# Performance work log

Measured on AMD Instinct MI355X. Metric: run time of the kernel, lower is better.

The kernel has to match this reference:

```python
import jax, jax.numpy as jnp
import numpy as np

ALPHA, BETA, GAMMA = 2.0, 2.0, 1.0
EPS = 1e-8  # torch F.cosine_similarity eps
B, T, D = 64, 1024, 256


def setup_inputs() -> dict:
    key = jax.random.key(0)
    k1, k2, k3 = jax.random.split(key, 3)
    f_v = jax.random.normal(k1, (B, T, D), dtype=jnp.float32)
    f_a = jax.random.normal(k2, (B, T, D), dtype=jnp.float32)
    labels = jax.random.randint(k3, (B,), 0, 2, dtype=jnp.int64)
    return {"f_v": f_v, "f_a": f_a, "labels": labels}


def _normalize(x):
    n = jnp.sqrt(jnp.sum(x * x, axis=-1, keepdims=True))
    return x / jnp.maximum(n, EPS)


def reference(f_v, f_a, labels):
    b, t, _ = f_v.shape
    vn = _normalize(f_v)  # [B,T,D]
    an = _normalize(f_a)  # [B,T,D]

    # --- per-timestep aligned-pair term ---
    cos_bt = jnp.sum(vn * an, axis=-1)  # [B,T] cosine sim
    d_bt = 1.0 - cos_bt                  # cosine distance
    pos_mask = (labels == 0).astype(f_v.dtype)[:, None]  # [B,1]
    neg_mask = 1.0 - pos_mask
    loss_pos = ALPHA * jnp.sum(d_bt * pos_mask)
    cnt_pos = jnp.sum(pos_mask) * t
    loss_neg = BETA * jnp.sum((1.0 - d_bt) * neg_mask)  # (1-d) == cos
    cnt_neg = jnp.sum(neg_mask) * t

    # --- cross-sample term: for i != j, (1 - mean_t d_ij) = mean_t cos(v_i_t, a_j_t) ---
    cross_cos = jnp.einsum('itd,jtd->ij', vn, an) / t  # [B,B] mean over T
    offdiag = 1.0 - jnp.eye(b, dtype=f_v.dtype)
    loss_neg = loss_neg + GAMMA * jnp.sum(cross_cos * offdiag)
    cnt_neg = cnt_neg + b * (b - 1)

    loss = jnp.where(cnt_pos > 0, loss_pos / jnp.maximum(cnt_pos, 1.0), 0.0)
    loss = loss + jnp.where(cnt_neg > 0, loss_neg / jnp.maximum(cnt_neg, 1.0), 0.0)
    return loss
```

## Files before the change

### kernel.cpp

```cpp
#include <hip/hip_runtime.h>

constexpr int Bn = 64;
constexpr int Tn = 1024;
constexpr int Dn = 256;

constexpr int TPB  = 256;
constexpr int NBLK = Tn / 4;
constexpr int NBIN = 64;

using short8 = __attribute__((ext_vector_type(8))) short;
using f32x16 = __attribute__((ext_vector_type(16))) float;

__device__ __forceinline__ float dot4(const float4& a, const float4& b) {
    return a.x * b.x + a.y * b.y + a.z * b.z + a.w * b.w;
}

__device__ __forceinline__ unsigned int bfbits(float x) {
    unsigned int u = __builtin_bit_cast(unsigned int, x);
    return (u + 0x7FFFu + ((u >> 16) & 1u)) >> 16;
}
__device__ __forceinline__ unsigned int pack_bf2(float lo, float hi) {
    return bfbits(lo) | (bfbits(hi) << 16);
}

struct Ch { float4 v0[2], v1[2], a0[2], a1[2]; };

__global__ __launch_bounds__(TPB, 3)
void cmfm_main(const float* __restrict__ fv, const float* __restrict__ fa,
               const int* __restrict__ labels, float* __restrict__ acc)
{
    const int lane = threadIdx.x & 63;
    const int wave = threadIdx.x >> 6;
    const int t    = blockIdx.x * 4 + wave;

    const int mrow = lane & 31;
    const int half = lane >> 5;

    const size_t RS = (size_t)Tn * Dn;
    const float* pv0 = fv + ((size_t)mrow * Tn + t) * Dn + half * 8;
    const float* pv1 = pv0 + 32 * RS;
    const float* pa0 = fa + ((size_t)mrow * Tn + t) * Dn + half * 8;
    const float* pa1 = pa0 + 32 * RS;

    f32x16 C00, C01, C10, C11;
    #pragma unroll
    for (int r = 0; r < 16; ++r) { C00[r] = 0.f; C01[r] = 0.f; C10[r] = 0.f; C11[r] = 0.f; }

    float sqv0 = 0.f, sqv1 = 0.f, sqa0 = 0.f, sqa1 = 0.f, dva0 = 0.f, dva1 = 0.f;

    #define LOADC(ch, OFF) do {                                              \
        ch.v0[0] = *reinterpret_cast<const float4*>(pv0 + (OFF));            \
        ch.v0[1] = *reinterpret_cast<const float4*>(pv0 + (OFF) + 4);        \
        ch.v1[0] = *reinterpret_cast<const float4*>(pv1 + (OFF));            \
        ch.v1[1] = *reinterpret_cast<const float4*>(pv1 + (OFF) + 4);        \
        ch.a0[0] = *reinterpret_cast<const float4*>(pa0 + (OFF));            \
        ch.a0[1] = *reinterpret_cast<const float4*>(pa0 + (OFF) + 4);        \
        ch.a1[0] = *reinterpret_cast<const float4*>(pa1 + (OFF));            \
        ch.a1[1] = *reinterpret_cast<const float4*>(pa1 + (OFF) + 4);        \
    } while (0)

    #define CONSUME(ch) do {                                                 \
        sqv0 += dot4(ch.v0[0], ch.v0[0]) + dot4(ch.v0[1], ch.v0[1]);         \
        sqv1 += dot4(ch.v1[0], ch.v1[0]) + dot4(ch.v1[1], ch.v1[1]);         \
        sqa0 += dot4(ch.a0[0], ch.a0[0]) + dot4(ch.a0[1], ch.a0[1]);         \
        sqa1 += dot4(ch.a1[0], ch.a1[0]) + dot4(ch.a1[1], ch.a1[1]);         \
        dva0 += dot4(ch.v0[0], ch.a0[0]) + dot4(ch.v0[1], ch.a0[1]);         \
        dva1 += dot4(ch.v1[0], ch.a1[0]) + dot4(ch.v1[1], ch.a1[1]);         \
        union { short8 s8; uint4 u4; } vf0, vf1, af0, af1;                   \
        vf0.u4.x = pack_bf2(ch.v0[0].x, ch.v0[0].y);                         \
        vf0.u4.y = pack_bf2(ch.v0[0].z, ch.v0[0].w);                         \
        vf0.u4.z = pack_bf2(ch.v0[1].x, ch.v0[1].y);                         \
        vf0.u4.w = pack_bf2(ch.v0[1].z, ch.v0[1].w);                         \
        vf1.u4.x = pack_bf2(ch.v1[0].x, ch.v1[0].y);                         \
        vf1.u4.y = pack_bf2(ch.v1[0].z, ch.v1[0].w);                         \
        vf1.u4.z = pack_bf2(ch.v1[1].x, ch.v1[1].y);                         \
        vf1.u4.w = pack_bf2(ch.v1[1].z, ch.v1[1].w);                         \
        af0.u4.x = pack_bf2(ch.a0[0].x, ch.a0[0].y);                         \
        af0.u4.y = pack_bf2(ch.a0[0].z, ch.a0[0].w);                         \
        af0.u4.z = pack_bf2(ch.a0[1].x, ch.a0[1].y);                         \
        af0.u4.w = pack_bf2(ch.a0[1].z, ch.a0[1].w);                         \
        af1.u4.x = pack_bf2(ch.a1[0].x, ch.a1[0].y);                         \
        af1.u4.y = pack_bf2(ch.a1[0].z, ch.a1[0].w);                         \
        af1.u4.z = pack_bf2(ch.a1[1].x, ch.a1[1].y);                         \
        af1.u4.w = pack_bf2(ch.a1[1].z, ch.a1[1].w);                         \
        C00 = __builtin_amdgcn_mfma_f32_32x32x16_bf16(vf0.s8, af0.s8, C00, 0, 0, 0); \
        C01 = __builtin_amdgcn_mfma_f32_32x32x16_bf16(vf0.s8, af1.s8, C01, 0, 0, 0); \
        C10 = __builtin_amdgcn_mfma_f32_32x32x16_bf16(vf1.s8, af0.s8, C10, 0, 0, 0); \
        C11 = __builtin_amdgcn_mfma_f32_32x32x16_bf16(vf1.s8, af1.s8, C11, 0, 0, 0); \
    } while (0)

    Ch cA, cB;
    LOADC(cA, 0);
    #pragma unroll 1
    for (int c = 0; c < Dn / 16; c += 2) {
        LOADC(cB, (c + 1) * 16);
        CONSUME(cA);
        if (c + 2 < Dn / 16) LOADC(cA, (c + 2) * 16);
        CONSUME(cB);
    }
    #undef LOADC
    #undef CONSUME

    sqv0 += __shfl_xor(sqv0, 32);  sqv1 += __shfl_xor(sqv1, 32);
    sqa0 += __shfl_xor(sqa0, 32);  sqa1 += __shfl_xor(sqa1, 32);
    dva0 += __shfl_xor(dva0, 32);  dva1 += __shfl_xor(dva1, 32);
    const float rv0 = 1.f / fmaxf(sqrtf(sqv0), 1e-8f);
    const float rv1 = 1.f / fmaxf(sqrtf(sqv1), 1e-8f);
    const float ra0 = 1.f / fmaxf(sqrtf(sqa0), 1e-8f);
    const float ra1 = 1.f / fmaxf(sqrtf(sqa1), 1e-8f);

    float pos = 0.f, neg = 0.f;
    if (half == 0) {
        const float c0 = dva0 * rv0 * ra0;
        const float c1 = dva1 * rv1 * ra1;
        if (labels[mrow] == 0)      pos += 1.f - c0; else neg += c0;
        if (labels[mrow + 32] == 0) pos += 1.f - c1; else neg += c1;
    }

    float od = 0.f;
    #define TILE(Cxx, RV, RA, EXCL) do {                                     \
        _Pragma("unroll")                                                    \
        for (int r = 0; r < 16; ++r) {                                       \
            const int ri = (r & 3) + 8 * (r >> 2) + 4 * half;                \
            const float rvi = __shfl(RV, ri);                                \
            float cc = Cxx[r];                                               \
            if (EXCL && ri == mrow) cc = 0.f;                                \
            od += rvi * (RA) * cc;                                           \
        }                                                                    \
    } while (0)
    TILE(C00, rv0, ra0, true);
    TILE(C01, rv0, ra1, false);
    TILE(C10, rv1, ra0, false);
    TILE(C11, rv1, ra1, true);
    #undef TILE

    #pragma unroll
    for (int off = 1; off < 64; off <<= 1) {
        pos += __shfl_xor(pos, off);
        neg += __shfl_xor(neg, off);
        od  += __shfl_xor(od, off);
    }
    if (lane == 0) {
        float* bin = acc + (size_t)(t & (NBIN - 1)) * 4;
        atomicAdd(bin + 0, pos);
        atomicAdd(bin + 1, neg);
        atomicAdd(bin + 2, od);
    }
}

__global__ void cmfm_final(const int* __restrict__ labels, const float* __restrict__ acc,
                           float* __restrict__ out) {
    const int l = threadIdx.x;
    float p = acc[l * 4 + 0];
    float n = acc[l * 4 + 1];
    float o = acc[l * 4 + 2];
    float npf = (labels[l] == 0) ? 1.f : 0.f;
    #pragma unroll
    for (int off = 1; off < 64; off <<= 1) {
        p += __shfl_xor(p, off);
        n += __shfl_xor(n, off);
        o += __shfl_xor(o, off);
        npf += __shfl_xor(npf, off);
    }
    if (l == 0) {
        const int np = (int)(npf + 0.5f);
        const float cnt_pos = (float)np * (float)Tn;
        const float cnt_neg = (float)(Bn - np) * (float)Tn + (float)Bn * (float)(Bn - 1);
        float loss = 0.f;
        if (np > 0) loss += 2.0f * p / cnt_pos;
        loss += (2.0f * n + 1.0f * o / (float)Tn) / cnt_neg;
        out[0] = loss;
    }
}

extern "C" void kernel_launch(void* const* d_in, const int* in_sizes, int n_in,
                              void* d_out, int out_size, void* d_ws, size_t ws_size,
                              hipStream_t stream) {
    const float* fv     = (const float*)d_in[0];
    const float* fa     = (const float*)d_in[1];
    const int*   labels = (const int*)d_in[2];
    float* acc = (float*)d_ws;
    float* out = (float*)d_out;

    hipMemsetAsync(acc, 0, NBIN * 4 * sizeof(float), stream);
    cmfm_main<<<NBLK, TPB, 0, stream>>>(fv, fa, labels, acc);
    cmfm_final<<<1, 64, 0, stream>>>(labels, acc, out);
}
```

Before: 169.7 us.

## Split D reduction across four waves per timestep, combine norms via shared memory

Each block now handles a single timestep, and its four waves each take a 64-wide slice of the feature dimension instead of each wave owning a whole timestep. Partial squared norms and dot products go to shared memory and are summed there. Each wave then applies the combined norms to its partial cross-sample MFMA tile, and the block reduces the results before the atomic adds. This gives four times as many blocks and shorter per-wave dependency chains to raise parallelism and latency hiding, at the cost of two block barriers and shared-memory traffic.

```diff
diff --git a/kernel.cpp b/kernel.cpp
--- a/kernel.cpp
+++ b/kernel.cpp
@@ -5,7 +5,7 @@
 constexpr int Dn = 256;
 
 constexpr int TPB  = 256;
-constexpr int NBLK = Tn / 4;
+constexpr int NBLK = Tn;
 constexpr int NBIN = 64;
 
 using short8 = __attribute__((ext_vector_type(8))) short;
@@ -29,17 +29,21 @@
 void cmfm_main(const float* __restrict__ fv, const float* __restrict__ fa,
                const int* __restrict__ labels, float* __restrict__ acc)
 {
+    __shared__ float nv[4][Bn], na[4][Bn], nd[4][Bn];
+    __shared__ float wred[3][4];
+
     const int lane = threadIdx.x & 63;
     const int wave = threadIdx.x >> 6;
-    const int t    = blockIdx.x * 4 + wave;
+    const int t    = blockIdx.x;
 
     const int mrow = lane & 31;
     const int half = lane >> 5;
 
     const size_t RS = (size_t)Tn * Dn;
-    const float* pv0 = fv + ((size_t)mrow * Tn + t) * Dn + half * 8;
+    const int koff  = wave * 64 + half * 8;
+    const float* pv0 = fv + ((size_t)mrow * Tn + t) * Dn + koff;
     const float* pv1 = pv0 + 32 * RS;
-    const float* pa0 = fa + ((size_t)mrow * Tn + t) * Dn + half * 8;
+    const float* pa0 = fa + ((size_t)mrow * Tn + t) * Dn + koff;
     const float* pa1 = pa0 + 32 * RS;
 
     f32x16 C00, C01, C10, C11;
@@ -92,10 +96,10 @@
     Ch cA, cB;
     LOADC(cA, 0);
     #pragma unroll 1
-    for (int c = 0; c < Dn / 16; c += 2) {
+    for (int c = 0; c < 4; c += 2) {
         LOADC(cB, (c + 1) * 16);
         CONSUME(cA);
-        if (c + 2 < Dn / 16) LOADC(cA, (c + 2) * 16);
+        if (c + 2 < 4) LOADC(cA, (c + 2) * 16);
         CONSUME(cB);
     }
     #undef LOADC
@@ -104,15 +108,28 @@
     sqv0 += __shfl_xor(sqv0, 32);  sqv1 += __shfl_xor(sqv1, 32);
     sqa0 += __shfl_xor(sqa0, 32);  sqa1 += __shfl_xor(sqa1, 32);
     dva0 += __shfl_xor(dva0, 32);  dva1 += __shfl_xor(dva1, 32);
-    const float rv0 = 1.f / fmaxf(sqrtf(sqv0), 1e-8f);
-    const float rv1 = 1.f / fmaxf(sqrtf(sqv1), 1e-8f);
-    const float ra0 = 1.f / fmaxf(sqrtf(sqa0), 1e-8f);
-    const float ra1 = 1.f / fmaxf(sqrtf(sqa1), 1e-8f);
+    if (half == 0) {
+        nv[wave][mrow] = sqv0;  nv[wave][mrow + 32] = sqv1;
+        na[wave][mrow] = sqa0;  na[wave][mrow + 32] = sqa1;
+        nd[wave][mrow] = dva0;  nd[wave][mrow + 32] = dva1;
+    }
+    __syncthreads();
+
+    const float fv0 = nv[0][mrow]      + nv[1][mrow]      + nv[2][mrow]      + nv[3][mrow];
+    const float fv1 = nv[0][mrow + 32] + nv[1][mrow + 32] + nv[2][mrow + 32] + nv[3][mrow + 32];
+    const float fa0 = na[0][mrow]      + na[1][mrow]      + na[2][mrow]      + na[3][mrow];
+    const float fa1 = na[0][mrow + 32] + na[1][mrow + 32] + na[2][mrow + 32] + na[3][mrow + 32];
+    const float rv0 = 1.f / fmaxf(sqrtf(fv0), 1e-8f);
+    const float rv1 = 1.f / fmaxf(sqrtf(fv1), 1e-8f);
+    const float ra0 = 1.f / fmaxf(sqrtf(fa0), 1e-8f);
+    const float ra1 = 1.f / fmaxf(sqrtf(fa1), 1e-8f);
 
     float pos = 0.f, neg = 0.f;
-    if (half == 0) {
-        const float c0 = dva0 * rv0 * ra0;
-        const float c1 = dva1 * rv1 * ra1;
+    if (wave == 0 && half == 0) {
+        const float fd0 = nd[0][mrow]      + nd[1][mrow]      + nd[2][mrow]      + nd[3][mrow];
+        const float fd1 = nd[0][mrow + 32] + nd[1][mrow + 32] + nd[2][mrow + 32] + nd[3][mrow + 32];
+        const float c0 = fd0 * rv0 * ra0;
+        const float c1 = fd1 * rv1 * ra1;
         if (labels[mrow] == 0)      pos += 1.f - c0; else neg += c0;
         if (labels[mrow + 32] == 0) pos += 1.f - c1; else neg += c1;
     }
@@ -140,11 +157,16 @@
         neg += __shfl_xor(neg, off);
         od  += __shfl_xor(od, off);
     }
-    if (lane == 0) {
+    if (lane == 0) { wred[0][wave] = pos; wred[1][wave] = neg; wred[2][wave] = od; }
+    __syncthreads();
+    if (threadIdx.x == 0) {
+        float p = 0.f, n = 0.f, o = 0.f;
+        #pragma unroll
+        for (int w = 0; w < 4; ++w) { p += wred[0][w]; n += wred[1][w]; o += wred[2][w]; }
         float* bin = acc + (size_t)(t & (NBIN - 1)) * 4;
-        atomicAdd(bin + 0, pos);
-        atomicAdd(bin + 1, neg);
-        atomicAdd(bin + 2, od);
+        atomicAdd(bin + 0, p);
+        atomicAdd(bin + 1, n);
+        atomicAdd(bin + 2, o);
     }
 }
 
```

Result: slower. 182.7 us (+7.7%).
